# Kernel optimization log

Hardware: AMD Instinct MI355X
Metric: run time of the kernel (lower is better)

## Reference

```python
import jax, jax.numpy as jnp
import numpy as np

G = 128        # number of graphs
N = 512        # nodes per graph
F_IN = 128     # n_feat
H = 128        # agg_hidden
L = 5          # n_layer
FC = 128       # fc_hidden
C = 10         # n_class
E_HALF = 8192  # undirected edge pairs per graph (symmetrized -> 16384 directed)


def setup_inputs() -> dict:
    key = jax.random.key(0)
    ks = jax.random.split(key, 8)
    x = jax.random.normal(ks[0], (G * N, F_IN), dtype=jnp.float32)
    # per-graph random edges, offset into the block-diagonal node index space
    s = jax.random.randint(ks[1], (G, E_HALF), 0, N)
    d = jax.random.randint(ks[2], (G, E_HALF), 0, N)
    off = (jnp.arange(G) * N)[:, None]
    s = (s + off).reshape(-1)
    d = (d + off).reshape(-1)
    src = jnp.concatenate([s, d])  # symmetric adjacency (edges + reversed)
    dst = jnp.concatenate([d, s])
    eps = jnp.zeros((L,), jnp.float32)  # nn.Parameter(torch.zeros(n_layer))
    W = jax.random.normal(ks[3], (L, H, H), jnp.float32) / jnp.sqrt(H)
    b = jnp.zeros((L, H), jnp.float32)
    fc1_w = jax.random.normal(ks[4], (H, FC), jnp.float32) / jnp.sqrt(H)
    fc1_b = jnp.zeros((FC,), jnp.float32)
    fc2_w = jax.random.normal(ks[5], (FC, C), jnp.float32) / jnp.sqrt(FC)
    fc2_b = jnp.zeros((C,), jnp.float32)
    return {"x": x, "eps": eps, "W": W, "b": b,
            "fc1_w": fc1_w, "fc1_b": fc1_b, "fc2_w": fc2_w, "fc2_b": fc2_b,
            "src": src, "dst": dst}


def reference(x, eps, W, b, fc1_w, fc1_b, fc2_w, fc2_b, src, dst):
    n = x.shape[0]
    h = x
    for i in range(L):
        # sparse Adj @ h : gather along src, scatter-add to dst
        pooled = jax.ops.segment_sum(h[src], dst, num_segments=n)
        h = jax.nn.relu(((1.0 + eps[i]) * h + pooled) @ W[i] + b[i])
        # dropout p=0.0 / eval mode -> identity
    hg = h.reshape(G, N, -1).sum(axis=1)          # sum readout over nodes
    hg = jax.nn.relu(hg @ fc1_w + fc1_b)
    return jax.nn.softmax(hg @ fc2_w + fc2_b, axis=-1)
```

## Files before the change

### kernel.cpp

```cpp
#include <hip/hip_runtime.h>

#define NODES 65536
#define GNUM  128
#define NPG   512
#define FDIM  128

#define OFF_A   0u
#define OFF_WT  (16u<<20)
#define OFF_HTA (17u<<20)
#define OFF_HTB (33u<<20)

typedef short bf16x8 __attribute__((ext_vector_type(8)));
typedef float f32x4  __attribute__((ext_vector_type(4)));
typedef unsigned short u16;

#define GLB_AS __attribute__((address_space(1)))
#define LDS_AS __attribute__((address_space(3)))

static __device__ inline void gload16(const void* g, void* l) {
    __builtin_amdgcn_global_load_lds((const GLB_AS unsigned*)g,
                                     (LDS_AS unsigned*)l, 16, 0, 0);
}

static __device__ inline unsigned bf1(float x) {
    unsigned b = __float_as_uint(x);
    return (b + 0x7fffu + ((b >> 16) & 1u)) >> 16;
}
static __device__ inline unsigned pack_bf2(float x, float y) {
    return bf1(x) | (bf1(y) << 16);
}
static __device__ inline bf16x8 cvt8n(unsigned x) {
    union { bf16x8 v; unsigned u[4]; } r;
#pragma unroll
    for (int i = 0; i < 4; ++i) {
        float f0 = (float)((x >> (8 * i)) & 0xFu);
        float f1 = (float)((x >> (8 * i + 4)) & 0xFu);
        r.u[i] = (__float_as_uint(f0) >> 16) | (__float_as_uint(f1) & 0xffff0000u);
    }
    return r.v;
}

__global__ __launch_bounds__(256) void k_cvtT(const float* __restrict__ x,
                                              u16* __restrict__ hT) {
    __shared__ char Cs[128 * 144];
    int t = threadIdx.x;
    int m0 = blockIdx.x * 64;
    int g = m0 >> 9, ml0 = m0 & 511;
#pragma unroll
    for (int it = 0; it < 8; ++it) {
        int i = t + 256 * it;
        int nl = i >> 5, fq = i & 31;
        float4 v = *(const float4*)(x + (size_t)(m0 + nl) * FDIM + fq * 4);
        *(u16*)(Cs + (fq * 4 + 0) * 144 + nl * 2) = (u16)bf1(v.x);
        *(u16*)(Cs + (fq * 4 + 1) * 144 + nl * 2) = (u16)bf1(v.y);
        *(u16*)(Cs + (fq * 4 + 2) * 144 + nl * 2) = (u16)bf1(v.z);
        *(u16*)(Cs + (fq * 4 + 3) * 144 + nl * 2) = (u16)bf1(v.w);
    }
    __syncthreads();
    u16* hg = hT + (size_t)g * 65536 + ml0;
#pragma unroll
    for (int j = 0; j < 4; ++j) {
        int idx = t + 256 * j;
        int f = idx >> 3, piece = idx & 7;
        uint4 v = *(const uint4*)(Cs + f * 144 + piece * 16);
        *(uint4*)((char*)(hg + (size_t)f * 512) + piece * 16) = v;
    }
}

__global__ __launch_bounds__(256) void k_wt(const float* __restrict__ W,
                                            u16* __restrict__ wt) {
    int idx = blockIdx.x * 256 + threadIdx.x;
    int l = idx >> 14, r = idx & 16383;
    int n = r >> 7, k = r & 127;
    wt[idx] = (u16)bf1(W[(l << 14) + k * 128 + n]);
}

__global__ __launch_bounds__(1024) void k_adense(const int* __restrict__ src,
                                                 const int* __restrict__ dst,
                                                 unsigned* __restrict__ A4,
                                                 int halfE) {
    __shared__ uint4 cnt4[512 * 16];
    unsigned* cnt = (unsigned*)cnt4;
    int g = blockIdx.x;
    int t = threadIdx.x;
#pragma unroll
    for (int j = 0; j < 8; ++j) cnt4[t + 1024 * j] = make_uint4(0u, 0u, 0u, 0u);
    __syncthreads();
    int epg = halfE / GNUM;
#pragma unroll
    for (int r = 0; r < 2; ++r) {
        int base = r * halfE + g * epg;
        const int4* s4 = (const int4*)(src + base);
        const int4* d4 = (const int4*)(dst + base);
#pragma unroll
        for (int it = 0; it < 2; ++it) {
            int i = t + 1024 * it;
            int4 sv = s4[i], dv = d4[i];
            int s, d;
            s = sv.x & 511; d = dv.x & 511; atomicAdd(&cnt[d * 64 + (s >> 3)], 1u << ((s & 7) * 4));
            s = sv.y & 511; d = dv.y & 511; atomicAdd(&cnt[d * 64 + (s >> 3)], 1u << ((s & 7) * 4));
            s = sv.z & 511; d = dv.z & 511; atomicAdd(&cnt[d * 64 + (s >> 3)], 1u << ((s & 7) * 4));
            s = sv.w & 511; d = dv.w & 511; atomicAdd(&cnt[d * 64 + (s >> 3)], 1u << ((s & 7) * 4));
        }
    }
    __syncthreads();
    uint4* Ao = (uint4*)(A4 + (size_t)g * 512 * 64);
#pragma unroll
    for (int j = 0; j < 8; ++j) Ao[t + 1024 * j] = cnt4[t + 1024 * j];
}

__global__ __launch_bounds__(256, 2) void k_layer(const u16* __restrict__ hT,
                                                  u16* __restrict__ hTo,
                                                  const unsigned char* __restrict__ A,
                                                  const u16* __restrict__ wt,
                                                  const float* __restrict__ bias,
                                                  const float* __restrict__ eps) {
    __shared__ uint4 smem16[61440 / 16];
    char* smem = (char*)smem16;
    char* Ps = smem + 12288;
    int t = threadIdx.x;
    int w = t >> 6, lane = t & 63;
    int q = lane >> 4, ln = lane & 15;
    int g = blockIdx.x & 127, dq = blockIdx.x >> 7;
    const unsigned char* Ab = A + (size_t)g * (512 * 256) + (size_t)dq * 128 * 256;
    const u16* hb = hT + (size_t)g * 65536;

    int pA = t;
    const unsigned char* gA = Ab + (pA >> 1) * 256 + (pA & 1) * 16;
    f32x4 acc[2][8];
#pragma unroll
    for (int mt = 0; mt < 2; ++mt)
#pragma unroll
        for (int nt = 0; nt < 8; ++nt) acc[mt][nt] = (f32x4){0.f, 0.f, 0.f, 0.f};

#pragma unroll
    for (int c = 0; c < 2; ++c) {
        gload16(gA + c * 32, smem + c * 4096 + pA * 16);
#pragma unroll
        for (int j = 0; j < 4; ++j) {
            int p = t + 256 * j; int f = p >> 3;
            gload16((const char*)hb + (size_t)f * 1024 + c * 128
                        + (((p & 7) ^ (f & 7)) << 4),
                    smem + 12288 + c * 16384 + p * 16);
        }
    }
    int rA0 = w * 32 + ln;
#pragma unroll
    for (int ch = 0; ch < 8; ++ch) {
        char* Asc = smem + (ch % 3) * 4096;
        char* Bsc = smem + 12288 + (ch % 3) * 16384;
        if (ch + 2 < 8) {
            int cn = ch + 2;
            char* Asn = smem + (cn % 3) * 4096;
            char* Bsn = smem + 12288 + (cn % 3) * 16384;
            gload16(gA + cn * 32, Asn + pA * 16);
#pragma unroll
            for (int j = 0; j < 4; ++j) {
                int p = t + 256 * j; int f = p >> 3;
                gload16((const char*)hb + (size_t)f * 1024 + cn * 128
                            + (((p & 7) ^ (f & 7)) << 4),
                        Bsn + p * 16);
            }
        }
        if (ch < 6)      asm volatile("s_waitcnt vmcnt(10)" ::: "memory");
        else if (ch < 7) asm volatile("s_waitcnt vmcnt(5)" ::: "memory");
        else             asm volatile("s_waitcnt vmcnt(0)" ::: "memory");
        __builtin_amdgcn_s_barrier();
#pragma unroll
        for (int kcL = 0; kcL < 2; ++kcL) {
            bf16x8 af0 = cvt8n(*(const unsigned*)(Asc + rA0 * 32 + kcL * 16 + q * 4));
            bf16x8 af1 = cvt8n(*(const unsigned*)(Asc + (rA0 + 16) * 32 + kcL * 16 + q * 4));
#pragma unroll
            for (int nt = 0; nt < 8; ++nt) {
                int f = nt * 16 + ln;
                int sB = f * 8 + ((kcL * 4 + q) ^ (f & 7));
                bf16x8 bf = *(const bf16x8*)(Bsc + sB * 16);
                acc[0][nt] = __builtin_amdgcn_mfma_f32_16x16x32_bf16(af0, bf, acc[0][nt], 0, 0, 0);
                acc[1][nt] = __builtin_amdgcn_mfma_f32_16x16x32_bf16(af1, bf, acc[1][nt], 0, 0, 0);
            }
        }
        __builtin_amdgcn_s_barrier();
    }
    float ep = 1.f + eps[0];
#pragma unroll
    for (int mt = 0; mt < 2; ++mt) {
        int rl0 = w * 32 + mt * 16 + q * 4;
        int mb0 = dq * 128 + rl0;
#pragma unroll
        for (int nt = 0; nt < 8; ++nt) {
            int f = nt * 16 + ln;
            uint2 sv = *(const uint2*)(hb + (size_t)f * 512 + mb0);
            float s0 = __uint_as_float(sv.x << 16);
            float s1 = __uint_as_float(sv.x & 0xffff0000u);
            float s2 = __uint_as_float(sv.y << 16);
            float s3 = __uint_as_float(sv.y & 0xffff0000u);
            f32x4 a = acc[mt][nt];
            *(u16*)(Ps + (rl0 + 0) * 272 + f * 2) = (u16)bf1(fmaf(ep, s0, a[0]));
            *(u16*)(Ps + (rl0 + 1) * 272 + f * 2) = (u16)bf1(fmaf(ep, s1, a[1]));
            *(u16*)(Ps + (rl0 + 2) * 272 + f * 2) = (u16)bf1(fmaf(ep, s2, a[2]));
            *(u16*)(Ps + (rl0 + 3) * 272 + f * 2) = (u16)bf1(fmaf(ep, s3, a[3]));
        }
    }
    __syncthreads();
    f32x4 acc2[2][8];
#pragma unroll
    for (int mt = 0; mt < 2; ++mt)
#pragma unroll
        for (int nt = 0; nt < 8; ++nt) acc2[mt][nt] = (f32x4){0.f, 0.f, 0.f, 0.f};
#pragma unroll
    for (int ks = 0; ks < 4; ++ks) {
        bf16x8 af0 = *(const bf16x8*)(Ps + rA0 * 272 + ks * 64 + q * 16);
        bf16x8 af1 = *(const bf16x8*)(Ps + (rA0 + 16) * 272 + ks * 64 + q * 16);
#pragma unroll
        for (int nt = 0; nt < 8; ++nt) {
            bf16x8 bf = *(const bf16x8*)(wt + (size_t)(nt * 16 + ln) * 128 + ks * 32 + q * 8);
            acc2[0][nt] = __builtin_amdgcn_mfma_f32_16x16x32_bf16(af0, bf, acc2[0][nt], 0, 0, 0);
            acc2[1][nt] = __builtin_amdgcn_mfma_f32_16x16x32_bf16(af1, bf, acc2[1][nt], 0, 0, 0);
        }
    }
    __syncthreads();
#pragma unroll
    for (int mt = 0; mt < 2; ++mt) {
        int rl0 = w * 32 + mt * 16 + q * 4;
#pragma unroll
        for (int nt = 0; nt < 8; ++nt) {
            int n = nt * 16 + ln;
            float bv = bias[n];
            f32x4 a = acc2[mt][nt];
            *(uint2*)(Ps + n * 272 + rl0 * 2) =
                make_uint2(pack_bf2(fmaxf(a[0] + bv, 0.f), fmaxf(a[1] + bv, 0.f)),
                           pack_bf2(fmaxf(a[2] + bv, 0.f), fmaxf(a[3] + bv, 0.f)));
        }
    }
    __syncthreads();
    u16* ho = hTo + (size_t)g * 65536 + dq * 128;
#pragma unroll
    for (int j = 0; j < 8; ++j) {
        int idx = t + 256 * j;
        int f = idx >> 4, piece = idx & 15;
        uint4 v = *(const uint4*)(Ps + f * 272 + piece * 16);
        *(uint4*)((char*)(ho + (size_t)f * 512) + piece * 16) = v;
    }
}

__global__ __launch_bounds__(128) void k_r(const u16* __restrict__ hT,
                                           const float* __restrict__ fc1w,
                                           const float* __restrict__ fc1b,
                                           const float* __restrict__ fc2w,
                                           const float* __restrict__ fc2b,
                                           float* __restrict__ out) {
    __shared__ float hg[128], z[128], lg[10];
    int g = blockIdx.x, t = threadIdx.x;
    const uint4* row = (const uint4*)(hT + (size_t)g * 65536 + (size_t)t * 512);
    float acc = 0.f;
#pragma unroll 4
    for (int i = 0; i < 64; ++i) {
        uint4 u = row[i];
        acc += __uint_as_float(u.x << 16) + __uint_as_float(u.x & 0xffff0000u);
        acc += __uint_as_float(u.y << 16) + __uint_as_float(u.y & 0xffff0000u);
        acc += __uint_as_float(u.z << 16) + __uint_as_float(u.z & 0xffff0000u);
        acc += __uint_as_float(u.w << 16) + __uint_as_float(u.w & 0xffff0000u);
    }
    hg[t] = acc;
    __syncthreads();
    float a1 = fc1b[t];
#pragma unroll 4
    for (int k = 0; k < 128; ++k) a1 = fmaf(hg[k], fc1w[k * 128 + t], a1);
    z[t] = fmaxf(a1, 0.f);
    __syncthreads();
    if (t < 10) {
        float l2 = fc2b[t];
        for (int k = 0; k < 128; ++k) l2 = fmaf(z[k], fc2w[k * 10 + t], l2);
        lg[t] = l2;
    }
    __syncthreads();
    if (t < 10) {
        float m = lg[0];
        for (int c = 1; c < 10; ++c) m = fmaxf(m, lg[c]);
        float ssum = 0.f;
        for (int c = 0; c < 10; ++c) ssum += expf(lg[c] - m);
        out[g * 10 + t] = expf(lg[t] - m) / ssum;
    }
}

extern "C" void kernel_launch(void* const* d_in, const int* in_sizes, int n_in,
                              void* d_out, int out_size, void* d_ws, size_t ws_size,
                              hipStream_t stream) {
    const float* x    = (const float*)d_in[0];
    const float* eps  = (const float*)d_in[1];
    const float* W    = (const float*)d_in[2];
    const float* b    = (const float*)d_in[3];
    const float* fc1w = (const float*)d_in[4];
    const float* fc1b = (const float*)d_in[5];
    const float* fc2w = (const float*)d_in[6];
    const float* fc2b = (const float*)d_in[7];
    const int*   src  = (const int*)d_in[8];
    const int*   dst  = (const int*)d_in[9];
    int E = in_sizes[8];
    int halfE = E >> 1;

    char* ws  = (char*)d_ws;
    unsigned char* Abuf = (unsigned char*)(ws + OFF_A);
    u16*  wtb = (u16*)(ws + OFF_WT);
    u16*  hta = (u16*)(ws + OFF_HTA);
    u16*  htb = (u16*)(ws + OFF_HTB);
    float* out = (float*)d_out;

    k_cvtT<<<NODES / 64, 256, 0, stream>>>(x, hta);
    k_wt<<<5 * 128 * 128 / 256, 256, 0, stream>>>(W, wtb);
    k_adense<<<GNUM, 1024, 0, stream>>>(src, dst, (unsigned*)Abuf, halfE);

    u16* cur = hta;
    u16* nxt = htb;
    for (int l = 0; l < 5; ++l) {
        k_layer<<<GNUM * 4, 256, 0, stream>>>(cur, nxt, Abuf,
                                              wtb + l * 128 * 128, b + l * 128, eps + l);
        u16* tmp = cur; cur = nxt; nxt = tmp;
    }
    k_r<<<GNUM, 128, 0, stream>>>(cur, fc1w, fc1b, fc2w, fc2b, out);
}
```

Measured before the change: 245.6 us.

## Double layer tile to 256 rows, preload adjacency into registers, merge prep kernels

Each layer block now handles half a graph (256 destination rows) with 512 threads instead of a quarter graph with 256 threads. The same per-graph h tile is therefore streamed through LDS half as many times. The packed 4-bit adjacency fragments are loaded straight into 32 registers per thread at kernel start rather than staged through LDS each chunk, which shrinks the pipelined loads to the h tiles only. The input-conversion and weight-transpose kernels are merged into one launch. The costs are higher register and LDS use (about 116 KB of LDS) and a grid of only 256 blocks, which lowers occupancy and parallelism on the GPU.

Result: slower. 282.6 us (+15.0%).

```diff
diff --git a/kernel.cpp b/kernel.cpp
--- a/kernel.cpp
+++ b/kernel.cpp
@@ -1,6 +1,5 @@
 #include <hip/hip_runtime.h>
 
-#define NODES 65536
 #define GNUM  128
 #define NPG   512
 #define FDIM  128
@@ -40,11 +39,21 @@
     return r.v;
 }
 
-__global__ __launch_bounds__(256) void k_cvtT(const float* __restrict__ x,
-                                              u16* __restrict__ hT) {
+__global__ __launch_bounds__(256) void k_prep(const float* __restrict__ x,
+                                              u16* __restrict__ hT,
+                                              const float* __restrict__ W,
+                                              u16* __restrict__ wt) {
     __shared__ char Cs[128 * 144];
     int t = threadIdx.x;
-    int m0 = blockIdx.x * 64;
+    int bid = blockIdx.x;
+    if (bid >= 1024) {
+        int idx = (bid - 1024) * 256 + t;
+        int l = idx >> 14, r = idx & 16383;
+        int n = r >> 7, k = r & 127;
+        wt[idx] = (u16)bf1(W[(l << 14) + k * 128 + n]);
+        return;
+    }
+    int m0 = bid * 64;
     int g = m0 >> 9, ml0 = m0 & 511;
 #pragma unroll
     for (int it = 0; it < 8; ++it) {
@@ -67,14 +76,6 @@
     }
 }
 
-__global__ __launch_bounds__(256) void k_wt(const float* __restrict__ W,
-                                            u16* __restrict__ wt) {
-    int idx = blockIdx.x * 256 + threadIdx.x;
-    int l = idx >> 14, r = idx & 16383;
-    int n = r >> 7, k = r & 127;
-    wt[idx] = (u16)bf1(W[(l << 14) + k * 128 + n]);
-}
-
 __global__ __launch_bounds__(1024) void k_adense(const int* __restrict__ src,
                                                  const int* __restrict__ dst,
                                                  unsigned* __restrict__ A4,
@@ -109,24 +110,33 @@
     for (int j = 0; j < 8; ++j) Ao[t + 1024 * j] = cnt4[t + 1024 * j];
 }
 
-__global__ __launch_bounds__(256, 2) void k_layer(const u16* __restrict__ hT,
+__global__ __launch_bounds__(512, 2) void k_layer(const u16* __restrict__ hT,
                                                   u16* __restrict__ hTo,
                                                   const unsigned char* __restrict__ A,
                                                   const u16* __restrict__ wt,
                                                   const float* __restrict__ bias,
                                                   const float* __restrict__ eps) {
-    __shared__ uint4 smem16[61440 / 16];
+    __shared__ uint4 smem16[118784 / 16];
     char* smem = (char*)smem16;
-    char* Ps = smem + 12288;
+    char* Ps = smem + 49152;
     int t = threadIdx.x;
     int w = t >> 6, lane = t & 63;
     int q = lane >> 4, ln = lane & 15;
-    int g = blockIdx.x & 127, dq = blockIdx.x >> 7;
-    const unsigned char* Ab = A + (size_t)g * (512 * 256) + (size_t)dq * 128 * 256;
+    int g = blockIdx.x & 127, hf = blockIdx.x >> 7;
+    const unsigned char* Ab = A + (size_t)g * 131072 + (size_t)hf * 65536;
     const u16* hb = hT + (size_t)g * 65536;
-
-    int pA = t;
-    const unsigned char* gA = Ab + (pA >> 1) * 256 + (pA & 1) * 16;
+    int rA0 = w * 32 + ln;
+
+    unsigned aA[32];
+#pragma unroll
+    for (int ch = 0; ch < 8; ++ch)
+#pragma unroll
+        for (int kcL = 0; kcL < 2; ++kcL)
+#pragma unroll
+            for (int h = 0; h < 2; ++h)
+                aA[ch * 4 + kcL * 2 + h] = *(const unsigned*)
+                    (Ab + (size_t)(rA0 + h * 16) * 256 + ch * 32 + kcL * 16 + q * 4);
+
     f32x4 acc[2][8];
 #pragma unroll
     for (int mt = 0; mt < 2; ++mt)
@@ -134,42 +144,36 @@
         for (int nt = 0; nt < 8; ++nt) acc[mt][nt] = (f32x4){0.f, 0.f, 0.f, 0.f};
 
 #pragma unroll
-    for (int c = 0; c < 2; ++c) {
-        gload16(gA + c * 32, smem + c * 4096 + pA * 16);
-#pragma unroll
-        for (int j = 0; j < 4; ++j) {
-            int p = t + 256 * j; int f = p >> 3;
+    for (int c = 0; c < 2; ++c)
+#pragma unroll
+        for (int j = 0; j < 2; ++j) {
+            int p = t + 512 * j; int f = p >> 3;
             gload16((const char*)hb + (size_t)f * 1024 + c * 128
                         + (((p & 7) ^ (f & 7)) << 4),
-                    smem + 12288 + c * 16384 + p * 16);
-        }
-    }
-    int rA0 = w * 32 + ln;
+                    smem + c * 16384 + p * 16);
+        }
 #pragma unroll
     for (int ch = 0; ch < 8; ++ch) {
-        char* Asc = smem + (ch % 3) * 4096;
-        char* Bsc = smem + 12288 + (ch % 3) * 16384;
-        if (ch + 2 < 8) {
+        char* Bsc = smem + (ch % 3) * 16384;
+        if (ch < 6) {
             int cn = ch + 2;
-            char* Asn = smem + (cn % 3) * 4096;
-            char* Bsn = smem + 12288 + (cn % 3) * 16384;
-            gload16(gA + cn * 32, Asn + pA * 16);
-#pragma unroll
-            for (int j = 0; j < 4; ++j) {
-                int p = t + 256 * j; int f = p >> 3;
+            char* Bsn = smem + (cn % 3) * 16384;
+#pragma unroll
+            for (int j = 0; j < 2; ++j) {
+                int p = t + 512 * j; int f = p >> 3;
                 gload16((const char*)hb + (size_t)f * 1024 + cn * 128
                             + (((p & 7) ^ (f & 7)) << 4),
                         Bsn + p * 16);
             }
         }
-        if (ch < 6)      asm volatile("s_waitcnt vmcnt(10)" ::: "memory");
-        else if (ch < 7) asm volatile("s_waitcnt vmcnt(5)" ::: "memory");
+        if (ch < 6)      asm volatile("s_waitcnt vmcnt(4)" ::: "memory");
+        else if (ch < 7) asm volatile("s_waitcnt vmcnt(2)" ::: "memory");
         else             asm volatile("s_waitcnt vmcnt(0)" ::: "memory");
         __builtin_amdgcn_s_barrier();
 #pragma unroll
         for (int kcL = 0; kcL < 2; ++kcL) {
-            bf16x8 af0 = cvt8n(*(const unsigned*)(Asc + rA0 * 32 + kcL * 16 + q * 4));
-            bf16x8 af1 = cvt8n(*(const unsigned*)(Asc + (rA0 + 16) * 32 + kcL * 16 + q * 4));
+            bf16x8 af0 = cvt8n(aA[ch * 4 + kcL * 2 + 0]);
+            bf16x8 af1 = cvt8n(aA[ch * 4 + kcL * 2 + 1]);
 #pragma unroll
             for (int nt = 0; nt < 8; ++nt) {
                 int f = nt * 16 + ln;
@@ -185,7 +189,7 @@
 #pragma unroll
     for (int mt = 0; mt < 2; ++mt) {
         int rl0 = w * 32 + mt * 16 + q * 4;
-        int mb0 = dq * 128 + rl0;
+        int mb0 = hf * 256 + rl0;
 #pragma unroll
         for (int nt = 0; nt < 8; ++nt) {
             int f = nt * 16 + ln;
@@ -227,18 +231,18 @@
             int n = nt * 16 + ln;
             float bv = bias[n];
             f32x4 a = acc2[mt][nt];
-            *(uint2*)(Ps + n * 272 + rl0 * 2) =
+            *(uint2*)(Ps + n * 528 + rl0 * 2) =
                 make_uint2(pack_bf2(fmaxf(a[0] + bv, 0.f), fmaxf(a[1] + bv, 0.f)),
                            pack_bf2(fmaxf(a[2] + bv, 0.f), fmaxf(a[3] + bv, 0.f)));
         }
     }
     __syncthreads();
-    u16* ho = hTo + (size_t)g * 65536 + dq * 128;
+    u16* ho = hTo + (size_t)g * 65536 + hf * 256;
 #pragma unroll
     for (int j = 0; j < 8; ++j) {
-        int idx = t + 256 * j;
-        int f = idx >> 4, piece = idx & 15;
-        uint4 v = *(const uint4*)(Ps + f * 272 + piece * 16);
+        int idx = t + 512 * j;
+        int f = idx >> 5, piece = idx & 31;
+        uint4 v = *(const uint4*)(Ps + f * 528 + piece * 16);
         *(uint4*)((char*)(ho + (size_t)f * 512) + piece * 16) = v;
     }
 }
@@ -306,14 +310,13 @@
     u16*  htb = (u16*)(ws + OFF_HTB);
     float* out = (float*)d_out;
 
-    k_cvtT<<<NODES / 64, 256, 0, stream>>>(x, hta);
-    k_wt<<<5 * 128 * 128 / 256, 256, 0, stream>>>(W, wtb);
+    k_prep<<<1344, 256, 0, stream>>>(x, hta, W, wtb);
     k_adense<<<GNUM, 1024, 0, stream>>>(src, dst, (unsigned*)Abuf, halfE);
 
     u16* cur = hta;
     u16* nxt = htb;
     for (int l = 0; l < 5; ++l) {
-        k_layer<<<GNUM * 4, 256, 0, stream>>>(cur, nxt, Abuf,
+        k_layer<<<GNUM * 2, 512, 0, stream>>>(cur, nxt, Abuf,
                                               wtb + l * 128 * 128, b + l * 128, eps + l);
         u16* tmp = cur; cur = nxt; nxt = tmp;
     }
```

## Fuse preprocessing kernels and use 4-stage LDS ring in layer kernel

Applied to the files above, without the earlier changes.

Merges the three preprocessing kernels (feature transpose/convert, weight transpose, dense adjacency build) into one launch that dispatches on block index, removing two launch gaps. In the layer kernel, the A/B staging ring grows from 3 to 4 slots so the second barrier per chunk can be dropped, and s_setprio raises wave priority around the MFMA section. LDS use rises from 60KB to 80KB per block, which may reduce how many blocks fit per CU, and the fused preprocessing kernel uses 1024-thread blocks with larger transpose tiles.

After: 251.0 us. 1.02x slower.

```diff
diff --git a/kernel.cpp b/kernel.cpp
--- a/kernel.cpp
+++ b/kernel.cpp
@@ -1,6 +1,5 @@
 #include <hip/hip_runtime.h>
 
-#define NODES 65536
 #define GNUM  128
 #define NPG   512
 #define FDIM  128
@@ -40,73 +39,77 @@
     return r.v;
 }
 
-__global__ __launch_bounds__(256) void k_cvtT(const float* __restrict__ x,
-                                              u16* __restrict__ hT) {
-    __shared__ char Cs[128 * 144];
+__global__ __launch_bounds__(1024) void k_pre(const float* __restrict__ x,
+                                              u16* __restrict__ hT,
+                                              const float* __restrict__ W,
+                                              u16* __restrict__ wt,
+                                              const int* __restrict__ src,
+                                              const int* __restrict__ dst,
+                                              unsigned* __restrict__ A4,
+                                              int halfE) {
+    __shared__ uint4 sm[8192];
     int t = threadIdx.x;
-    int m0 = blockIdx.x * 64;
-    int g = m0 >> 9, ml0 = m0 & 511;
-#pragma unroll
-    for (int it = 0; it < 8; ++it) {
-        int i = t + 256 * it;
-        int nl = i >> 5, fq = i & 31;
-        float4 v = *(const float4*)(x + (size_t)(m0 + nl) * FDIM + fq * 4);
-        *(u16*)(Cs + (fq * 4 + 0) * 144 + nl * 2) = (u16)bf1(v.x);
-        *(u16*)(Cs + (fq * 4 + 1) * 144 + nl * 2) = (u16)bf1(v.y);
-        *(u16*)(Cs + (fq * 4 + 2) * 144 + nl * 2) = (u16)bf1(v.z);
-        *(u16*)(Cs + (fq * 4 + 3) * 144 + nl * 2) = (u16)bf1(v.w);
-    }
-    __syncthreads();
-    u16* hg = hT + (size_t)g * 65536 + ml0;
-#pragma unroll
-    for (int j = 0; j < 4; ++j) {
-        int idx = t + 256 * j;
-        int f = idx >> 3, piece = idx & 7;
-        uint4 v = *(const uint4*)(Cs + f * 144 + piece * 16);
-        *(uint4*)((char*)(hg + (size_t)f * 512) + piece * 16) = v;
-    }
-}
-
-__global__ __launch_bounds__(256) void k_wt(const float* __restrict__ W,
-                                            u16* __restrict__ wt) {
-    int idx = blockIdx.x * 256 + threadIdx.x;
-    int l = idx >> 14, r = idx & 16383;
-    int n = r >> 7, k = r & 127;
-    wt[idx] = (u16)bf1(W[(l << 14) + k * 128 + n]);
-}
-
-__global__ __launch_bounds__(1024) void k_adense(const int* __restrict__ src,
-                                                 const int* __restrict__ dst,
-                                                 unsigned* __restrict__ A4,
-                                                 int halfE) {
-    __shared__ uint4 cnt4[512 * 16];
-    unsigned* cnt = (unsigned*)cnt4;
-    int g = blockIdx.x;
-    int t = threadIdx.x;
-#pragma unroll
-    for (int j = 0; j < 8; ++j) cnt4[t + 1024 * j] = make_uint4(0u, 0u, 0u, 0u);
-    __syncthreads();
-    int epg = halfE / GNUM;
-#pragma unroll
-    for (int r = 0; r < 2; ++r) {
-        int base = r * halfE + g * epg;
-        const int4* s4 = (const int4*)(src + base);
-        const int4* d4 = (const int4*)(dst + base);
-#pragma unroll
-        for (int it = 0; it < 2; ++it) {
+    int bid = blockIdx.x;
+    if (bid < GNUM) {
+        unsigned* cnt = (unsigned*)sm;
+        int g = bid;
+#pragma unroll
+        for (int j = 0; j < 8; ++j) sm[t + 1024 * j] = make_uint4(0u, 0u, 0u, 0u);
+        __syncthreads();
+        int epg = halfE / GNUM;
+#pragma unroll
+        for (int r = 0; r < 2; ++r) {
+            int base = r * halfE + g * epg;
+            const int4* s4 = (const int4*)(src + base);
+            const int4* d4 = (const int4*)(dst + base);
+#pragma unroll
+            for (int it = 0; it < 2; ++it) {
+                int i = t + 1024 * it;
+                int4 sv = s4[i], dv = d4[i];
+                int s, d;
+                s = sv.x & 511; d = dv.x & 511; atomicAdd(&cnt[d * 64 + (s >> 3)], 1u << ((s & 7) * 4));
+                s = sv.y & 511; d = dv.y & 511; atomicAdd(&cnt[d * 64 + (s >> 3)], 1u << ((s & 7) * 4));
+                s = sv.z & 511; d = dv.z & 511; atomicAdd(&cnt[d * 64 + (s >> 3)], 1u << ((s & 7) * 4));
+                s = sv.w & 511; d = dv.w & 511; atomicAdd(&cnt[d * 64 + (s >> 3)], 1u << ((s & 7) * 4));
+            }
+        }
+        __syncthreads();
+        uint4* Ao = (uint4*)(A4 + (size_t)g * 512 * 64);
+#pragma unroll
+        for (int j = 0; j < 8; ++j) Ao[t + 1024 * j] = sm[t + 1024 * j];
+        return;
+    }
+    if (bid < GNUM + 256) {
+        char* Cs = (char*)sm;
+        int m0 = (bid - GNUM) * 256;
+        int g = m0 >> 9, ml0 = m0 & 511;
+#pragma unroll
+        for (int it = 0; it < 8; ++it) {
             int i = t + 1024 * it;
-            int4 sv = s4[i], dv = d4[i];
-            int s, d;
-            s = sv.x & 511; d = dv.x & 511; atomicAdd(&cnt[d * 64 + (s >> 3)], 1u << ((s & 7) * 4));
-            s = sv.y & 511; d = dv.y & 511; atomicAdd(&cnt[d * 64 + (s >> 3)], 1u << ((s & 7) * 4));
-            s = sv.z & 511; d = dv.z & 511; atomicAdd(&cnt[d * 64 + (s >> 3)], 1u << ((s & 7) * 4));
-            s = sv.w & 511; d = dv.w & 511; atomicAdd(&cnt[d * 64 + (s >> 3)], 1u << ((s & 7) * 4));
-        }
-    }
-    __syncthreads();
-    uint4* Ao = (uint4*)(A4 + (size_t)g * 512 * 64);
-#pragma unroll
-    for (int j = 0; j < 8; ++j) Ao[t + 1024 * j] = cnt4[t + 1024 * j];
+            int nl = i >> 5, fq = i & 31;
+            float4 v = *(const float4*)(x + (size_t)(m0 + nl) * FDIM + fq * 4);
+            *(u16*)(Cs + (fq * 4 + 0) * 528 + nl * 2) = (u16)bf1(v.x);
+            *(u16*)(Cs + (fq * 4 + 1) * 528 + nl * 2) = (u16)bf1(v.y);
+            *(u16*)(Cs + (fq * 4 + 2) * 528 + nl * 2) = (u16)bf1(v.z);
+            *(u16*)(Cs + (fq * 4 + 3) * 528 + nl * 2) = (u16)bf1(v.w);
+        }
+        __syncthreads();
+        u16* hg = hT + (size_t)g * 65536 + ml0;
+#pragma unroll
+        for (int j = 0; j < 4; ++j) {
+            int idx = t + 1024 * j;
+            int f = idx >> 5, piece = idx & 31;
+            uint4 v = *(const uint4*)(Cs + f * 528 + piece * 16);
+            *(uint4*)((char*)(hg + (size_t)f * 512) + piece * 16) = v;
+        }
+        return;
+    }
+    {
+        int idx = (bid - GNUM - 256) * 1024 + t;
+        int l = idx >> 14, r = idx & 16383;
+        int n = r >> 7, k = r & 127;
+        wt[idx] = (u16)bf1(W[(l << 14) + k * 128 + n]);
+    }
 }
 
 __global__ __launch_bounds__(256, 2) void k_layer(const u16* __restrict__ hT,
@@ -115,14 +118,14 @@
                                                   const u16* __restrict__ wt,
                                                   const float* __restrict__ bias,
                                                   const float* __restrict__ eps) {
-    __shared__ uint4 smem16[61440 / 16];
+    __shared__ uint4 smem16[81920 / 16];
     char* smem = (char*)smem16;
-    char* Ps = smem + 12288;
+    char* Ps = smem;
     int t = threadIdx.x;
     int w = t >> 6, lane = t & 63;
     int q = lane >> 4, ln = lane & 15;
     int g = blockIdx.x & 127, dq = blockIdx.x >> 7;
-    const unsigned char* Ab = A + (size_t)g * (512 * 256) + (size_t)dq * 128 * 256;
+    const unsigned char* Ab = A + (size_t)g * 131072 + (size_t)dq * 32768;
     const u16* hb = hT + (size_t)g * 65536;
 
     int pA = t;
@@ -141,18 +144,18 @@
             int p = t + 256 * j; int f = p >> 3;
             gload16((const char*)hb + (size_t)f * 1024 + c * 128
                         + (((p & 7) ^ (f & 7)) << 4),
-                    smem + 12288 + c * 16384 + p * 16);
+                    smem + 16384 + c * 16384 + p * 16);
         }
     }
     int rA0 = w * 32 + ln;
 #pragma unroll
     for (int ch = 0; ch < 8; ++ch) {
-        char* Asc = smem + (ch % 3) * 4096;
-        char* Bsc = smem + 12288 + (ch % 3) * 16384;
-        if (ch + 2 < 8) {
+        char* Asc = smem + (ch & 3) * 4096;
+        char* Bsc = smem + 16384 + (ch & 3) * 16384;
+        if (ch < 6) {
             int cn = ch + 2;
-            char* Asn = smem + (cn % 3) * 4096;
-            char* Bsn = smem + 12288 + (cn % 3) * 16384;
+            char* Asn = smem + (cn & 3) * 4096;
+            char* Bsn = smem + 16384 + (cn & 3) * 16384;
             gload16(gA + cn * 32, Asn + pA * 16);
 #pragma unroll
             for (int j = 0; j < 4; ++j) {
@@ -166,6 +169,7 @@
         else if (ch < 7) asm volatile("s_waitcnt vmcnt(5)" ::: "memory");
         else             asm volatile("s_waitcnt vmcnt(0)" ::: "memory");
         __builtin_amdgcn_s_barrier();
+        __builtin_amdgcn_s_setprio(1);
 #pragma unroll
         for (int kcL = 0; kcL < 2; ++kcL) {
             bf16x8 af0 = cvt8n(*(const unsigned*)(Asc + rA0 * 32 + kcL * 16 + q * 4));
@@ -179,8 +183,9 @@
                 acc[1][nt] = __builtin_amdgcn_mfma_f32_16x16x32_bf16(af1, bf, acc[1][nt], 0, 0, 0);
             }
         }
-        __builtin_amdgcn_s_barrier();
-    }
+        __builtin_amdgcn_s_setprio(0);
+    }
+    __builtin_amdgcn_s_barrier();
     float ep = 1.f + eps[0];
 #pragma unroll
     for (int mt = 0; mt < 2; ++mt) {
@@ -306,9 +311,8 @@
     u16*  htb = (u16*)(ws + OFF_HTB);
     float* out = (float*)d_out;
 
-    k_cvtT<<<NODES / 64, 256, 0, stream>>>(x, hta);
-    k_wt<<<5 * 128 * 128 / 256, 256, 0, stream>>>(W, wtb);
-    k_adense<<<GNUM, 1024, 0, stream>>>(src, dst, (unsigned*)Abuf, halfE);
+    k_pre<<<GNUM + 256 + 80, 1024, 0, stream>>>(x, hta, W, wtb, src, dst,
+                                                (unsigned*)Abuf, halfE);
 
     u16* cur = hta;
     u16* nxt = htb;
```
